# Optimization experiments

Measured on AMD Instinct MI355X. Metric: run time of the kernel, lower is better.

## Reference

```python
import jax, jax.numpy as jnp
import numpy as np

EPS = 1e-5
THRESH = 1.5


def _compute_one(x, g_w, g_b, phi_w, phi_b, W_w, W_b, gamma, beta):
    # x: (c, w, h, z) -- single sample (torch code calls compute_x with batch 1)
    c, w, h, z = x.shape
    nz = z // 2
    # AdaptiveAvgPool3d(1) on x.permute(0,4,2,3,1): mean over (w, h, c) per z-slice -> (z,)
    p = x.mean(axis=(0, 1, 2))
    xp = x * p[None, None, None, :]
    # 1x1x1 conv projections (note: self.theta is defined but unused in the original)
    g_x = jnp.einsum('ic,cwhz->iwhz', g_w, x) + g_b[:, None, None, None]
    phi_x = jnp.einsum('ic,cwhz->iwhz', phi_w, xp) + phi_b[:, None, None, None]
    # MaxPool3d kernel (1,1,2): non-overlapping max pairs along z
    g_x = g_x.reshape(-1, w, h, nz, 2).max(axis=-1)      # (ic, w, h, nz)
    phi_x = phi_x.reshape(-1, w, h, nz, 2).max(axis=-1)  # (ic, w, h, nz)
    # theta_x: (x*p).permute(0,2,3,4,1).view(w*h, z, c)
    theta = xp.transpose(1, 2, 3, 0).reshape(w * h, z, c)
    # phi: permute(0,2,3,1,4).view(w*h, ic, nz)
    phi_m = phi_x.transpose(1, 2, 0, 3).reshape(w * h, -1, nz)
    # g: permute(0,2,3,4,1).view(w*h, nz, ic)
    g_m = g_x.transpose(1, 2, 3, 0).reshape(w * h, nz, -1)
    f = jnp.einsum('bzc,bcn->bzn', theta, phi_m)          # (wh, z, nz)
    a = jax.nn.softmax(f, axis=-1)
    y = jnp.einsum('bzn,bni->bzi', a, g_m)                # (wh, z, ic)
    y = y.reshape(w, h, z, -1).transpose(3, 0, 1, 2)      # (ic, w, h, z)
    wy = jnp.einsum('ci,iwhz->cwhz', W_w, y) + W_b[:, None, None, None]
    # BatchNorm3d in training mode on a single-sample batch: per-channel stats over (w,h,z)
    mu = wy.mean(axis=(1, 2, 3), keepdims=True)
    var = wy.var(axis=(1, 2, 3), keepdims=True)
    wy = (wy - mu) * jax.lax.rsqrt(var + EPS)
    wy = wy * gamma[:, None, None, None] + beta[:, None, None, None]
    return wy + x


def setup_inputs() -> dict:
    key = jax.random.key(0)
    ks = jax.random.split(key, 10)
    b, c, w, h, z = 2, 64, 64, 64, 64
    ic = c  # inter_channels defaults to in_channels
    x = jax.random.normal(ks[0], (b, c, w, h, z), dtype=jnp.float32)
    # spacings in [0, 3): some samples fall above spacing_thresh=1.5 (identity branch)
    spacings = jax.random.uniform(ks[1], (b, 3), dtype=jnp.float32) * 3.0
    g_w = jax.random.normal(ks[2], (ic, c), dtype=jnp.float32) * 0.1
    g_b = jax.random.normal(ks[3], (ic,), dtype=jnp.float32) * 0.1
    phi_w = jax.random.normal(ks[4], (ic, c), dtype=jnp.float32) * 0.1
    phi_b = jax.random.normal(ks[5], (ic,), dtype=jnp.float32) * 0.1
    W_w = jax.random.normal(ks[6], (c, ic), dtype=jnp.float32) * 0.1
    W_b = jax.random.normal(ks[7], (c,), dtype=jnp.float32) * 0.1
    gamma = jax.random.normal(ks[8], (c,), dtype=jnp.float32) * 0.1
    beta = jax.random.normal(ks[9], (c,), dtype=jnp.float32) * 0.1
    return {"x": x, "spacings": spacings, "g_w": g_w, "g_b": g_b,
            "phi_w": phi_w, "phi_b": phi_b, "W_w": W_w, "W_b": W_b,
            "gamma": gamma, "beta": beta}


def reference(x, spacings, g_w, g_b, phi_w, phi_b, W_w, W_b, gamma, beta):
    out = jax.vmap(_compute_one, in_axes=(0,) + (None,) * 8)(
        x, g_w, g_b, phi_w, phi_b, W_w, W_b, gamma, beta)
    use = (spacings[:, -1] <= THRESH)[:, None, None, None, None]
    return jnp.where(use, out, x)
```

## Files before the change

kernel.cpp:

```cpp
#include <hip/hip_runtime.h>
#include <math.h>

#define THRESH_SP 1.5f
#define WHZc   262144
#define CWHZc  16777216

#define WS_PSUM   0
#define WS_SLOT   128
#define WS_ZERO_N 8320
#define WS_WY_BYTE 65536
#define WS_WY_NEED (WS_WY_BYTE + 2u * CWHZc * 2u)

typedef __attribute__((ext_vector_type(8))) short bf16x8;
typedef __attribute__((ext_vector_type(4))) float floatx4;

#define MFMA(a, b, c) __builtin_amdgcn_mfma_f32_16x16x32_bf16((a), (b), (c), 0, 0, 0)

__device__ __forceinline__ unsigned short f2b(float f) {
    unsigned int u = __builtin_bit_cast(unsigned int, f);
    return (unsigned short)((u + 0x7FFFu + ((u >> 16) & 1u)) >> 16);
}
__device__ __forceinline__ float b2f(unsigned short h) {
    unsigned int u = ((unsigned int)h) << 16;
    return __builtin_bit_cast(float, u);
}
__device__ __forceinline__ bf16x8 ldfrag(const unsigned short* p, int elem_off) {
    return *(const bf16x8*)(p + elem_off);
}

__global__ __launch_bounds__(256) void k_zero(float* __restrict__ ws) {
    int i = blockIdx.x * blockDim.x + threadIdx.x;
    if (i < WS_ZERO_N) ws[i] = 0.0f;
}

__global__ __launch_bounds__(256) void k_pmean(const float* __restrict__ x,
                                               const float* __restrict__ sp,
                                               float* __restrict__ ws) {
    const int b = blockIdx.x >> 9;
    if (sp[b*3 + 2] > THRESH_SP) return;
    const int jb = blockIdx.x & 511;
    __shared__ float s[64];
    const int t = threadIdx.x;
    if (t < 64) s[t] = 0.0f;
    __syncthreads();
    const int idx4 = jb * 256 + t;
    const int z0 = (idx4 & 15) * 4;
    float a0 = 0.f, a1 = 0.f, a2 = 0.f, a3 = 0.f;
    const float* xb = x + (size_t)b * CWHZc;
#pragma unroll 4
    for (int it = 0; it < 32; ++it) {
        const float4 v = *(const float4*)&xb[(size_t)(idx4 + it * 131072) * 4];
        a0 += v.x; a1 += v.y; a2 += v.z; a3 += v.w;
    }
    a0 += __shfl_xor(a0, 16); a0 += __shfl_xor(a0, 32);
    a1 += __shfl_xor(a1, 16); a1 += __shfl_xor(a1, 32);
    a2 += __shfl_xor(a2, 16); a2 += __shfl_xor(a2, 32);
    a3 += __shfl_xor(a3, 16); a3 += __shfl_xor(a3, 32);
    if ((t & 63) < 16) {
        unsafeAtomicAdd(&s[z0 + 0], a0);
        unsafeAtomicAdd(&s[z0 + 1], a1);
        unsafeAtomicAdd(&s[z0 + 2], a2);
        unsafeAtomicAdd(&s[z0 + 3], a3);
    }
    __syncthreads();
    if (t < 64) unsafeAtomicAdd(&ws[WS_PSUM + b * 64 + t], s[t]);
}

__global__ __launch_bounds__(256, 4) void k_main(
    const float* __restrict__ x, const float* __restrict__ sp,
    const float* __restrict__ gw, const float* __restrict__ gb,
    const float* __restrict__ pw, const float* __restrict__ pb,
    const float* __restrict__ Wwp, const float* __restrict__ Wbp,
    float* __restrict__ out, unsigned short* __restrict__ wy16, int use16,
    float* __restrict__ ws) {
    const int blk = blockIdx.x;
    const int b = blk >> 12;
    if (sp[b*3 + 2] > THRESH_SP) return;
    const int wh = blk & 4095;
    const int xbase = b * CWHZc + wh * 64;

    __shared__ unsigned short xT[64 * 72];
    __shared__ unsigned short wb[64 * 72];
    __shared__ unsigned short gpT[64 * 40];
    __shared__ unsigned short phpN[32 * 72];
    __shared__ unsigned short aT[64 * 40];
    __shared__ float p_s[64];

    const int t  = threadIdx.x;
    const int l  = t & 63;
    const int lr = l & 15;
    const int lq = l >> 4;
    const int zt = (t >> 6) << 4;

#pragma unroll
    for (int k = 0; k < 4; ++k) {
        const int f = t + (k << 8);
        const int c = f & 63, zq = f >> 6;
        const float4 v = *(const float4*)&x[xbase + c * WHZc + zq * 4];
        xT[(zq*4 + 0)*72 + c] = f2b(v.x);
        xT[(zq*4 + 1)*72 + c] = f2b(v.y);
        xT[(zq*4 + 2)*72 + c] = f2b(v.z);
        xT[(zq*4 + 3)*72 + c] = f2b(v.w);
    }
#pragma unroll
    for (int k = 0; k < 4; ++k) {
        const int f = t + (k << 8);
        const int i = f >> 4, c4 = f & 15;
        const float4 v = *(const float4*)&gw[i*64 + c4*4];
        uint2 pk;
        pk.x = (unsigned int)f2b(v.x) | ((unsigned int)f2b(v.y) << 16);
        pk.y = (unsigned int)f2b(v.z) | ((unsigned int)f2b(v.w) << 16);
        *(uint2*)&wb[i*72 + c4*4] = pk;
    }
    if (t < 64) p_s[t] = ws[WS_PSUM + b*64 + t] * (1.0f / 262144.0f);
    __syncthreads();

    const bf16x8 a0 = ldfrag(xT, (zt + lr)*72 + lq*8);
    const bf16x8 a1 = ldfrag(xT, (zt + lr)*72 + lq*8 + 32);
    const float pz0 = p_s[zt + lq*4 + 0], pz1 = p_s[zt + lq*4 + 1];
    const float pz2 = p_s[zt + lq*4 + 2], pz3 = p_s[zt + lq*4 + 3];

    {
        const int n0 = (zt >> 1) + lq*2;
#pragma unroll
        for (int ti = 0; ti < 4; ++ti) {
            const int i = ti*16 + lr;
            const float bv = gb[i];
            floatx4 acc = {bv, bv, bv, bv};
            acc = MFMA(a0, ldfrag(wb, i*72 + lq*8), acc);
            acc = MFMA(a1, ldfrag(wb, i*72 + lq*8 + 32), acc);
            unsigned int pk = (unsigned int)f2b(fmaxf(acc[0], acc[1])) |
                              ((unsigned int)f2b(fmaxf(acc[2], acc[3])) << 16);
            *(unsigned int*)&gpT[i*40 + n0] = pk;
        }
    }
    __syncthreads();

#pragma unroll
    for (int k = 0; k < 4; ++k) {
        const int f = t + (k << 8);
        const int i = f >> 4, c4 = f & 15;
        const float4 v = *(const float4*)&pw[i*64 + c4*4];
        uint2 pk;
        pk.x = (unsigned int)f2b(v.x) | ((unsigned int)f2b(v.y) << 16);
        pk.y = (unsigned int)f2b(v.z) | ((unsigned int)f2b(v.w) << 16);
        *(uint2*)&wb[i*72 + c4*4] = pk;
    }
    __syncthreads();

    {
        const int n0 = (zt >> 1) + lq*2;
#pragma unroll
        for (int ti = 0; ti < 4; ++ti) {
            const int i = ti*16 + lr;
            floatx4 acc = {0.f, 0.f, 0.f, 0.f};
            acc = MFMA(a0, ldfrag(wb, i*72 + lq*8), acc);
            acc = MFMA(a1, ldfrag(wb, i*72 + lq*8 + 32), acc);
            const float bv = pb[i];
            const float v0 = fmaf(acc[0], pz0, bv), v1 = fmaf(acc[1], pz1, bv);
            const float v2 = fmaf(acc[2], pz2, bv), v3 = fmaf(acc[3], pz3, bv);
            phpN[n0*72 + i]       = f2b(fmaxf(v0, v1));
            phpN[(n0 + 1)*72 + i] = f2b(fmaxf(v2, v3));
        }
    }
    __syncthreads();

    {
        floatx4 f0 = {0.f, 0.f, 0.f, 0.f}, f1 = {0.f, 0.f, 0.f, 0.f};
        f0 = MFMA(a0, ldfrag(phpN, lr*72 + lq*8), f0);
        f0 = MFMA(a1, ldfrag(phpN, lr*72 + lq*8 + 32), f0);
        f1 = MFMA(a0, ldfrag(phpN, (16 + lr)*72 + lq*8), f1);
        f1 = MFMA(a1, ldfrag(phpN, (16 + lr)*72 + lq*8 + 32), f1);
        const float pz[4] = {pz0, pz1, pz2, pz3};
#pragma unroll
        for (int r = 0; r < 4; ++r) {
            const float fr0 = f0[r] * pz[r], fr1 = f1[r] * pz[r];
            float m = fmaxf(fr0, fr1);
            m = fmaxf(m, __shfl_xor(m, 1)); m = fmaxf(m, __shfl_xor(m, 2));
            m = fmaxf(m, __shfl_xor(m, 4)); m = fmaxf(m, __shfl_xor(m, 8));
            const float e0 = __expf(fr0 - m), e1 = __expf(fr1 - m);
            float s = e0 + e1;
            s += __shfl_xor(s, 1); s += __shfl_xor(s, 2);
            s += __shfl_xor(s, 4); s += __shfl_xor(s, 8);
            const float inv = 1.0f / s;
            const int z = zt + lq*4 + r;
            aT[z*40 + lr]      = f2b(e0 * inv);
            aT[z*40 + lr + 16] = f2b(e1 * inv);
        }
#pragma unroll
        for (int k = 0; k < 4; ++k) {
            const int f = t + (k << 8);
            const int i = f >> 4, c4 = f & 15;
            const float4 v = *(const float4*)&Wwp[i*64 + c4*4];
            uint2 pk;
            pk.x = (unsigned int)f2b(v.x) | ((unsigned int)f2b(v.y) << 16);
            pk.y = (unsigned int)f2b(v.z) | ((unsigned int)f2b(v.w) << 16);
            *(uint2*)&wb[i*72 + c4*4] = pk;
        }
    }
    __syncthreads();

    {
        float* statsf = (float*)phpN;
        if (t < 128) statsf[t] = 0.0f;
        const bf16x8 av = ldfrag(aT, (zt + lr)*40 + lq*8);
#pragma unroll
        for (int ti = 0; ti < 4; ++ti) {
            floatx4 acc = {0.f, 0.f, 0.f, 0.f};
            acc = MFMA(av, ldfrag(gpT, (ti*16 + lr)*40 + lq*8), acc);
#pragma unroll
            for (int r = 0; r < 4; ++r)
                xT[(zt + lq*4 + r)*72 + ti*16 + lr] = f2b(acc[r]);
        }
    }
    __syncthreads();

    {
        float* statsf = (float*)phpN;
        const bf16x8 y0 = ldfrag(xT, (zt + lr)*72 + lq*8);
        const bf16x8 y1 = ldfrag(xT, (zt + lr)*72 + lq*8 + 32);
#pragma unroll
        for (int ti = 0; ti < 4; ++ti) {
            const int co = ti*16 + lr;
            const float bv = Wbp[co];
            floatx4 acc = {bv, bv, bv, bv};
            acc = MFMA(y0, ldfrag(wb, co*72 + lq*8), acc);
            acc = MFMA(y1, ldfrag(wb, co*72 + lq*8 + 32), acc);
            if (use16) {
                uint2 pk;
                pk.x = (unsigned int)f2b(acc[0]) | ((unsigned int)f2b(acc[1]) << 16);
                pk.y = (unsigned int)f2b(acc[2]) | ((unsigned int)f2b(acc[3]) << 16);
                *(uint2*)&wy16[(size_t)xbase + co * WHZc + zt + lq*4] = pk;
            } else {
                *(float4*)&out[xbase + co * WHZc + zt + lq*4] = *(float4*)&acc;
            }
            float s1 = acc[0] + acc[1] + acc[2] + acc[3];
            float s2 = acc[0]*acc[0] + acc[1]*acc[1] + acc[2]*acc[2] + acc[3]*acc[3];
            s1 += __shfl_xor(s1, 16); s1 += __shfl_xor(s1, 32);
            s2 += __shfl_xor(s2, 16); s2 += __shfl_xor(s2, 32);
            if (lq == 0) {
                atomicAdd(&statsf[co*2],     s1);
                atomicAdd(&statsf[co*2 + 1], s2);
            }
        }
    }
    __syncthreads();
    {
        const float* statsf = (const float*)phpN;
        if (t < 128) {
            const int slot = blk & 31;
            unsafeAtomicAdd(&ws[WS_SLOT + (slot*2 + b)*128 + t], statsf[t]);
        }
    }
}

__global__ __launch_bounds__(256) void k_final(const float* __restrict__ x,
                                               const float* __restrict__ sp,
                                               const float* __restrict__ gamma,
                                               const float* __restrict__ beta,
                                               float* __restrict__ out,
                                               const unsigned short* __restrict__ wy16,
                                               int use16,
                                               const float* __restrict__ ws) {
    const bool use0 = sp[2] <= THRESH_SP;
    const bool use1 = sp[5] <= THRESH_SP;
    __shared__ float scf[128], shf[128];
    if ((use0 || use1) && threadIdx.x < 128) {
        const int t = threadIdx.x;
        const int b = t >> 6, c = t & 63;
        float S1 = 0.f, S2 = 0.f;
        for (int s = 0; s < 32; s++) {
            S1 += ws[WS_SLOT + (s*2 + b)*128 + c*2 + 0];
            S2 += ws[WS_SLOT + (s*2 + b)*128 + c*2 + 1];
        }
        const float N = 262144.0f;
        const float mu = S1 / N;
        const float var = fmaxf(S2 / N - mu * mu, 0.0f);
        const float sc = gamma[c] * rsqrtf(var + 1e-5f);
        scf[t] = sc;
        shf[t] = beta[c] - mu * sc;
    }
    __syncthreads();
    const int nf4 = (2 * CWHZc) / 4;
    for (int i4 = blockIdx.x * blockDim.x + threadIdx.x; i4 < nf4;
         i4 += gridDim.x * blockDim.x) {
        const int idx = i4 * 4;
        const int b = idx >> 24;
        const bool use = b ? use1 : use0;
        const float4 xv = *(const float4*)&x[idx];
        float4 ov;
        if (use) {
            const int c = (idx >> 18) & 63;
            const float scv = scf[b * 64 + c];
            const float shv = shf[b * 64 + c];
            float w0, w1, w2, w3;
            if (use16) {
                const uint2 q = *(const uint2*)&wy16[idx];
                w0 = b2f((unsigned short)(q.x & 0xffffu));
                w1 = b2f((unsigned short)(q.x >> 16));
                w2 = b2f((unsigned short)(q.y & 0xffffu));
                w3 = b2f((unsigned short)(q.y >> 16));
            } else {
                const float4 wy = *(const float4*)&out[idx];
                w0 = wy.x; w1 = wy.y; w2 = wy.z; w3 = wy.w;
            }
            ov.x = w0 * scv + shv + xv.x;
            ov.y = w1 * scv + shv + xv.y;
            ov.z = w2 * scv + shv + xv.z;
            ov.w = w3 * scv + shv + xv.w;
        } else {
            ov = xv;
        }
        *(float4*)&out[idx] = ov;
    }
}

extern "C" void kernel_launch(void* const* d_in, const int* in_sizes, int n_in,
                              void* d_out, int out_size, void* d_ws, size_t ws_size,
                              hipStream_t stream) {
    const float* x     = (const float*)d_in[0];
    const float* spv   = (const float*)d_in[1];
    const float* gw    = (const float*)d_in[2];
    const float* gb    = (const float*)d_in[3];
    const float* pw    = (const float*)d_in[4];
    const float* pb    = (const float*)d_in[5];
    const float* Ww    = (const float*)d_in[6];
    const float* Wb    = (const float*)d_in[7];
    const float* gamma = (const float*)d_in[8];
    const float* beta  = (const float*)d_in[9];
    float* out = (float*)d_out;
    float* ws  = (float*)d_ws;
    const int use16 = (ws_size >= (size_t)WS_WY_NEED) ? 1 : 0;
    unsigned short* wy16 = (unsigned short*)((char*)d_ws + WS_WY_BYTE);

    k_zero<<<(WS_ZERO_N + 255) / 256, 256, 0, stream>>>(ws);
    k_pmean<<<1024, 256, 0, stream>>>(x, spv, ws);
    k_main<<<8192, 256, 0, stream>>>(x, spv, gw, gb, pw, pb, Ww, Wb,
                                     out, wy16, use16, ws);
    k_final<<<2048, 256, 0, stream>>>(x, spv, gamma, beta, out, wy16, use16, ws);
}
```

Baseline: 130.6 us.

## Stage a bf16 copy of x in the mean pass and pre-convert weights

The channel-mean kernel now also writes a bf16 copy of x to the workspace. The main kernel loads its x tile from that copy, and the final kernel reads the residual x from it too, cutting fp32 traffic in later stages. A small prep kernel converts the three weight matrices to bf16 once, so each block copies them directly instead of converting per block. The trade-offs are an extra write pass over x and a residual add done in bf16 precision, which may widen output error. Each path is used only when the workspace is large enough.

```diff
diff --git a/kernel.cpp b/kernel.cpp
--- a/kernel.cpp
+++ b/kernel.cpp
@@ -1,4 +1,5 @@
 #include <hip/hip_runtime.h>
+#include <hip/hip_bf16.h>
 #include <math.h>
 
 #define THRESH_SP 1.5f
@@ -8,8 +9,12 @@
 #define WS_PSUM   0
 #define WS_SLOT   128
 #define WS_ZERO_N 8320
-#define WS_WY_BYTE 65536
-#define WS_WY_NEED (WS_WY_BYTE + 2u * CWHZc * 2u)
+#define WS_W16_BYTE  65536
+#define WS_WY_BYTE   131072
+#define WS_X16_BYTE  (WS_WY_BYTE + 2u*CWHZc*2u)
+#define WS_W16_NEED  (WS_W16_BYTE + 3u*4096u*2u)
+#define WS_WY_NEED   (WS_WY_BYTE + 2u*CWHZc*2u)
+#define WS_X16_NEED  (WS_X16_BYTE + 2u*CWHZc*2u)
 
 typedef __attribute__((ext_vector_type(8))) short bf16x8;
 typedef __attribute__((ext_vector_type(4))) float floatx4;
@@ -17,8 +22,8 @@
 #define MFMA(a, b, c) __builtin_amdgcn_mfma_f32_16x16x32_bf16((a), (b), (c), 0, 0, 0)
 
 __device__ __forceinline__ unsigned short f2b(float f) {
-    unsigned int u = __builtin_bit_cast(unsigned int, f);
-    return (unsigned short)((u + 0x7FFFu + ((u >> 16) & 1u)) >> 16);
+    __hip_bfloat16 h = __float2bfloat16(f);
+    return __builtin_bit_cast(unsigned short, h);
 }
 __device__ __forceinline__ float b2f(unsigned short h) {
     unsigned int u = ((unsigned int)h) << 16;
@@ -28,14 +33,26 @@
     return *(const bf16x8*)(p + elem_off);
 }
 
-__global__ __launch_bounds__(256) void k_zero(float* __restrict__ ws) {
-    int i = blockIdx.x * blockDim.x + threadIdx.x;
+__global__ __launch_bounds__(256) void k_prep(const float* __restrict__ gw,
+                                              const float* __restrict__ pw,
+                                              const float* __restrict__ Ww,
+                                              float* __restrict__ ws,
+                                              unsigned short* __restrict__ w16,
+                                              int usew16) {
+    const int i = blockIdx.x * 256 + threadIdx.x;
     if (i < WS_ZERO_N) ws[i] = 0.0f;
+    if (usew16 && i < 4096) {
+        w16[i]        = f2b(gw[i]);
+        w16[4096 + i] = f2b(pw[i]);
+        w16[8192 + i] = f2b(Ww[i]);
+    }
 }
 
 __global__ __launch_bounds__(256) void k_pmean(const float* __restrict__ x,
                                                const float* __restrict__ sp,
-                                               float* __restrict__ ws) {
+                                               float* __restrict__ ws,
+                                               unsigned short* __restrict__ x16,
+                                               int usex16) {
     const int b = blockIdx.x >> 9;
     if (sp[b*3 + 2] > THRESH_SP) return;
     const int jb = blockIdx.x & 511;
@@ -47,10 +64,18 @@
     const int z0 = (idx4 & 15) * 4;
     float a0 = 0.f, a1 = 0.f, a2 = 0.f, a3 = 0.f;
     const float* xb = x + (size_t)b * CWHZc;
+    unsigned short* xo = x16 + (size_t)b * CWHZc;
 #pragma unroll 4
     for (int it = 0; it < 32; ++it) {
-        const float4 v = *(const float4*)&xb[(size_t)(idx4 + it * 131072) * 4];
+        const size_t e4 = (size_t)(idx4 + it * 131072);
+        const float4 v = *(const float4*)&xb[e4 * 4];
         a0 += v.x; a1 += v.y; a2 += v.z; a3 += v.w;
+        if (usex16) {
+            uint2 pk;
+            pk.x = (unsigned int)f2b(v.x) | ((unsigned int)f2b(v.y) << 16);
+            pk.y = (unsigned int)f2b(v.z) | ((unsigned int)f2b(v.w) << 16);
+            *(uint2*)&xo[e4 * 4] = pk;
+        }
     }
     a0 += __shfl_xor(a0, 16); a0 += __shfl_xor(a0, 32);
     a1 += __shfl_xor(a1, 16); a1 += __shfl_xor(a1, 32);
@@ -72,6 +97,8 @@
     const float* __restrict__ pw, const float* __restrict__ pb,
     const float* __restrict__ Wwp, const float* __restrict__ Wbp,
     float* __restrict__ out, unsigned short* __restrict__ wy16, int use16,
+    const unsigned short* __restrict__ w16, int usew16,
+    const unsigned short* __restrict__ x16, int usex16,
     float* __restrict__ ws) {
     const int blk = blockIdx.x;
     const int b = blk >> 12;
@@ -92,25 +119,47 @@
     const int lq = l >> 4;
     const int zt = (t >> 6) << 4;
 
-#pragma unroll
-    for (int k = 0; k < 4; ++k) {
-        const int f = t + (k << 8);
-        const int c = f & 63, zq = f >> 6;
-        const float4 v = *(const float4*)&x[xbase + c * WHZc + zq * 4];
-        xT[(zq*4 + 0)*72 + c] = f2b(v.x);
-        xT[(zq*4 + 1)*72 + c] = f2b(v.y);
-        xT[(zq*4 + 2)*72 + c] = f2b(v.z);
-        xT[(zq*4 + 3)*72 + c] = f2b(v.w);
-    }
-#pragma unroll
-    for (int k = 0; k < 4; ++k) {
-        const int f = t + (k << 8);
-        const int i = f >> 4, c4 = f & 15;
-        const float4 v = *(const float4*)&gw[i*64 + c4*4];
-        uint2 pk;
-        pk.x = (unsigned int)f2b(v.x) | ((unsigned int)f2b(v.y) << 16);
-        pk.y = (unsigned int)f2b(v.z) | ((unsigned int)f2b(v.w) << 16);
-        *(uint2*)&wb[i*72 + c4*4] = pk;
+    if (usex16) {
+        const unsigned short* xs = x16 + xbase;
+#pragma unroll
+        for (int k = 0; k < 2; ++k) {
+            const int f = t + (k << 8);
+            const int c = f >> 3, seg = f & 7;
+            uint4 q = *(const uint4*)&xs[c * WHZc + seg * 8];
+            const unsigned short* qs = (const unsigned short*)&q;
+#pragma unroll
+            for (int j = 0; j < 8; ++j) xT[(seg*8 + j)*72 + c] = qs[j];
+        }
+    } else {
+#pragma unroll
+        for (int k = 0; k < 4; ++k) {
+            const int f = t + (k << 8);
+            const int c = f & 63, zq = f >> 6;
+            const float4 v = *(const float4*)&x[xbase + c * WHZc + zq * 4];
+            xT[(zq*4 + 0)*72 + c] = f2b(v.x);
+            xT[(zq*4 + 1)*72 + c] = f2b(v.y);
+            xT[(zq*4 + 2)*72 + c] = f2b(v.z);
+            xT[(zq*4 + 3)*72 + c] = f2b(v.w);
+        }
+    }
+    if (usew16) {
+#pragma unroll
+        for (int k = 0; k < 2; ++k) {
+            const int f = t + (k << 8);
+            const int i = f >> 3, seg = f & 7;
+            *(uint4*)&wb[i*72 + seg*8] = *(const uint4*)&w16[i*64 + seg*8];
+        }
+    } else {
+#pragma unroll
+        for (int k = 0; k < 4; ++k) {
+            const int f = t + (k << 8);
+            const int i = f >> 4, c4 = f & 15;
+            const float4 v = *(const float4*)&gw[i*64 + c4*4];
+            uint2 pk;
+            pk.x = (unsigned int)f2b(v.x) | ((unsigned int)f2b(v.y) << 16);
+            pk.y = (unsigned int)f2b(v.z) | ((unsigned int)f2b(v.w) << 16);
+            *(uint2*)&wb[i*72 + c4*4] = pk;
+        }
     }
     if (t < 64) p_s[t] = ws[WS_PSUM + b*64 + t] * (1.0f / 262144.0f);
     __syncthreads();
@@ -136,15 +185,24 @@
     }
     __syncthreads();
 
-#pragma unroll
-    for (int k = 0; k < 4; ++k) {
-        const int f = t + (k << 8);
-        const int i = f >> 4, c4 = f & 15;
-        const float4 v = *(const float4*)&pw[i*64 + c4*4];
-        uint2 pk;
-        pk.x = (unsigned int)f2b(v.x) | ((unsigned int)f2b(v.y) << 16);
-        pk.y = (unsigned int)f2b(v.z) | ((unsigned int)f2b(v.w) << 16);
-        *(uint2*)&wb[i*72 + c4*4] = pk;
+    if (usew16) {
+#pragma unroll
+        for (int k = 0; k < 2; ++k) {
+            const int f = t + (k << 8);
+            const int i = f >> 3, seg = f & 7;
+            *(uint4*)&wb[i*72 + seg*8] = *(const uint4*)&w16[4096 + i*64 + seg*8];
+        }
+    } else {
+#pragma unroll
+        for (int k = 0; k < 4; ++k) {
+            const int f = t + (k << 8);
+            const int i = f >> 4, c4 = f & 15;
+            const float4 v = *(const float4*)&pw[i*64 + c4*4];
+            uint2 pk;
+            pk.x = (unsigned int)f2b(v.x) | ((unsigned int)f2b(v.y) << 16);
+            pk.y = (unsigned int)f2b(v.z) | ((unsigned int)f2b(v.w) << 16);
+            *(uint2*)&wb[i*72 + c4*4] = pk;
+        }
     }
     __syncthreads();
 
@@ -187,15 +245,24 @@
             aT[z*40 + lr]      = f2b(e0 * inv);
             aT[z*40 + lr + 16] = f2b(e1 * inv);
         }
-#pragma unroll
-        for (int k = 0; k < 4; ++k) {
-            const int f = t + (k << 8);
-            const int i = f >> 4, c4 = f & 15;
-            const float4 v = *(const float4*)&Wwp[i*64 + c4*4];
-            uint2 pk;
-            pk.x = (unsigned int)f2b(v.x) | ((unsigned int)f2b(v.y) << 16);
-            pk.y = (unsigned int)f2b(v.z) | ((unsigned int)f2b(v.w) << 16);
-            *(uint2*)&wb[i*72 + c4*4] = pk;
+        if (usew16) {
+#pragma unroll
+            for (int k = 0; k < 2; ++k) {
+                const int f = t + (k << 8);
+                const int i = f >> 3, seg = f & 7;
+                *(uint4*)&wb[i*72 + seg*8] = *(const uint4*)&w16[8192 + i*64 + seg*8];
+            }
+        } else {
+#pragma unroll
+            for (int k = 0; k < 4; ++k) {
+                const int f = t + (k << 8);
+                const int i = f >> 4, c4 = f & 15;
+                const float4 v = *(const float4*)&Wwp[i*64 + c4*4];
+                uint2 pk;
+                pk.x = (unsigned int)f2b(v.x) | ((unsigned int)f2b(v.y) << 16);
+                pk.y = (unsigned int)f2b(v.z) | ((unsigned int)f2b(v.w) << 16);
+                *(uint2*)&wb[i*72 + c4*4] = pk;
+            }
         }
     }
     __syncthreads();
@@ -261,6 +328,8 @@
                                                float* __restrict__ out,
                                                const unsigned short* __restrict__ wy16,
                                                int use16,
+                                               const unsigned short* __restrict__ x16,
+                                               int usex16,
                                                const float* __restrict__ ws) {
     const bool use0 = sp[2] <= THRESH_SP;
     const bool use1 = sp[5] <= THRESH_SP;
@@ -287,12 +356,22 @@
         const int idx = i4 * 4;
         const int b = idx >> 24;
         const bool use = b ? use1 : use0;
-        const float4 xv = *(const float4*)&x[idx];
         float4 ov;
         if (use) {
             const int c = (idx >> 18) & 63;
             const float scv = scf[b * 64 + c];
             const float shv = shf[b * 64 + c];
+            float x0, x1, x2, x3;
+            if (usex16) {
+                const uint2 q = *(const uint2*)&x16[idx];
+                x0 = b2f((unsigned short)(q.x & 0xffffu));
+                x1 = b2f((unsigned short)(q.x >> 16));
+                x2 = b2f((unsigned short)(q.y & 0xffffu));
+                x3 = b2f((unsigned short)(q.y >> 16));
+            } else {
+                const float4 xv = *(const float4*)&x[idx];
+                x0 = xv.x; x1 = xv.y; x2 = xv.z; x3 = xv.w;
+            }
             float w0, w1, w2, w3;
             if (use16) {
                 const uint2 q = *(const uint2*)&wy16[idx];
@@ -304,12 +383,12 @@
                 const float4 wy = *(const float4*)&out[idx];
                 w0 = wy.x; w1 = wy.y; w2 = wy.z; w3 = wy.w;
             }
-            ov.x = w0 * scv + shv + xv.x;
-            ov.y = w1 * scv + shv + xv.y;
-            ov.z = w2 * scv + shv + xv.z;
-            ov.w = w3 * scv + shv + xv.w;
+            ov.x = w0 * scv + shv + x0;
+            ov.y = w1 * scv + shv + x1;
+            ov.z = w2 * scv + shv + x2;
+            ov.w = w3 * scv + shv + x3;
         } else {
-            ov = xv;
+            ov = *(const float4*)&x[idx];
         }
         *(float4*)&out[idx] = ov;
     }
@@ -330,12 +409,17 @@
     const float* beta  = (const float*)d_in[9];
     float* out = (float*)d_out;
     float* ws  = (float*)d_ws;
-    const int use16 = (ws_size >= (size_t)WS_WY_NEED) ? 1 : 0;
+    const int usew16 = (ws_size >= (size_t)WS_W16_NEED) ? 1 : 0;
+    const int use16  = (ws_size >= (size_t)WS_WY_NEED) ? 1 : 0;
+    const int usex16 = (ws_size >= (size_t)WS_X16_NEED) ? 1 : 0;
+    unsigned short* w16  = (unsigned short*)((char*)d_ws + WS_W16_BYTE);
     unsigned short* wy16 = (unsigned short*)((char*)d_ws + WS_WY_BYTE);
-
-    k_zero<<<(WS_ZERO_N + 255) / 256, 256, 0, stream>>>(ws);
-    k_pmean<<<1024, 256, 0, stream>>>(x, spv, ws);
+    unsigned short* x16  = (unsigned short*)((char*)d_ws + WS_X16_BYTE);
+
+    k_prep<<<48, 256, 0, stream>>>(gw, pw, Ww, ws, w16, usew16);
+    k_pmean<<<1024, 256, 0, stream>>>(x, spv, ws, x16, usex16);
     k_main<<<8192, 256, 0, stream>>>(x, spv, gw, gb, pw, pb, Ww, Wb,
-                                     out, wy16, use16, ws);
-    k_final<<<2048, 256, 0, stream>>>(x, spv, gamma, beta, out, wy16, use16, ws);
-}
+                                     out, wy16, use16, w16, usew16, x16, usex16, ws);
+    k_final<<<2048, 256, 0, stream>>>(x, spv, gamma, beta, out, wy16, use16,
+                                      x16, usex16, ws);
+}
```

After: 141.2 us. 1.08x slower.

## Process two wh columns per block sharing pre-converted bf16 weights in LDS

Applied to the files above, without the earlier changes.

Weights for g, phi and W are converted to bf16 once in a prep kernel, and each 512-thread block of k_main now handles two wh positions that share the weight tiles in LDS. The phi weights get their own buffer, which removes one barrier, and the W weights are loaded during the softmax phase to overlap with compute. Biases are staged in shared memory. The aim is to cut redundant weight conversion and loading and to reduce synchronisation. The cost is higher LDS use per block (about 61 KB), which may limit how many blocks fit on a CU.

```diff
diff --git a/kernel.cpp b/kernel.cpp
--- a/kernel.cpp
+++ b/kernel.cpp
@@ -1,4 +1,5 @@
 #include <hip/hip_runtime.h>
+#include <hip/hip_bf16.h>
 #include <math.h>
 
 #define THRESH_SP 1.5f
@@ -8,8 +9,10 @@
 #define WS_PSUM   0
 #define WS_SLOT   128
 #define WS_ZERO_N 8320
-#define WS_WY_BYTE 65536
-#define WS_WY_NEED (WS_WY_BYTE + 2u * CWHZc * 2u)
+#define WS_W16_BYTE  65536
+#define WS_WY_BYTE   131072
+#define WS_W16_NEED  (WS_W16_BYTE + 3u*4096u*2u)
+#define WS_WY_NEED   (WS_WY_BYTE + 2u*CWHZc*2u)
 
 typedef __attribute__((ext_vector_type(8))) short bf16x8;
 typedef __attribute__((ext_vector_type(4))) float floatx4;
@@ -17,8 +20,8 @@
 #define MFMA(a, b, c) __builtin_amdgcn_mfma_f32_16x16x32_bf16((a), (b), (c), 0, 0, 0)
 
 __device__ __forceinline__ unsigned short f2b(float f) {
-    unsigned int u = __builtin_bit_cast(unsigned int, f);
-    return (unsigned short)((u + 0x7FFFu + ((u >> 16) & 1u)) >> 16);
+    __hip_bfloat16 h = __float2bfloat16(f);
+    return __builtin_bit_cast(unsigned short, h);
 }
 __device__ __forceinline__ float b2f(unsigned short h) {
     unsigned int u = ((unsigned int)h) << 16;
@@ -28,9 +31,19 @@
     return *(const bf16x8*)(p + elem_off);
 }
 
-__global__ __launch_bounds__(256) void k_zero(float* __restrict__ ws) {
-    int i = blockIdx.x * blockDim.x + threadIdx.x;
+__global__ __launch_bounds__(256) void k_prep(const float* __restrict__ gw,
+                                              const float* __restrict__ pw,
+                                              const float* __restrict__ Ww,
+                                              float* __restrict__ ws,
+                                              unsigned short* __restrict__ w16,
+                                              int usew16) {
+    const int i = blockIdx.x * 256 + threadIdx.x;
     if (i < WS_ZERO_N) ws[i] = 0.0f;
+    if (usew16 && i < 4096) {
+        w16[i]        = f2b(gw[i]);
+        w16[4096 + i] = f2b(pw[i]);
+        w16[8192 + i] = f2b(Ww[i]);
+    }
 }
 
 __global__ __launch_bounds__(256) void k_pmean(const float* __restrict__ x,
@@ -66,35 +79,59 @@
     if (t < 64) unsafeAtomicAdd(&ws[WS_PSUM + b * 64 + t], s[t]);
 }
 
-__global__ __launch_bounds__(256, 4) void k_main(
+#define L_WG     0
+#define L_WP     9216
+#define L_XA     18432
+#define L_GPA    27648
+#define L_PHA    32768
+#define L_XB     37376
+#define L_GPB    46592
+#define L_PHB    51712
+#define L_ATB    56320
+#define L_BIAS   61440
+#define L_PS     62208
+#define L_TOTAL  62464
+
+__global__ __launch_bounds__(512, 4) void k_main(
     const float* __restrict__ x, const float* __restrict__ sp,
     const float* __restrict__ gw, const float* __restrict__ gb,
     const float* __restrict__ pw, const float* __restrict__ pb,
     const float* __restrict__ Wwp, const float* __restrict__ Wbp,
     float* __restrict__ out, unsigned short* __restrict__ wy16, int use16,
+    const unsigned short* __restrict__ w16, int usew16,
     float* __restrict__ ws) {
     const int blk = blockIdx.x;
-    const int b = blk >> 12;
+    const int b = blk >> 11;
     if (sp[b*3 + 2] > THRESH_SP) return;
-    const int wh = blk & 4095;
+    const int whpair = (blk & 2047) * 2;
+
+    __shared__ char smem[L_TOTAL];
+    unsigned short* wg   = (unsigned short*)(smem + L_WG);
+    unsigned short* wp   = (unsigned short*)(smem + L_WP);
+    float*          bias = (float*)(smem + L_BIAS);
+    float*          p_s  = (float*)(smem + L_PS);
+    float*          statsf = (float*)(smem + L_PHA);
+
+    const int t   = threadIdx.x;
+    const int wv  = t >> 6;
+    const int cid = wv >> 2;
+    const int tt  = t & 255;
+    const int l   = t & 63;
+    const int lr  = l & 15;
+    const int lq  = l >> 4;
+    const int zt  = (wv & 3) << 4;
+
+    unsigned short* xT   = (unsigned short*)(smem + (cid ? L_XB  : L_XA));
+    unsigned short* gpT  = (unsigned short*)(smem + (cid ? L_GPB : L_GPA));
+    unsigned short* phpN = (unsigned short*)(smem + (cid ? L_PHB : L_PHA));
+    unsigned short* aT   = (unsigned short*)(smem + (cid ? L_ATB : L_WG));
+
+    const int wh    = whpair + cid;
     const int xbase = b * CWHZc + wh * 64;
 
-    __shared__ unsigned short xT[64 * 72];
-    __shared__ unsigned short wb[64 * 72];
-    __shared__ unsigned short gpT[64 * 40];
-    __shared__ unsigned short phpN[32 * 72];
-    __shared__ unsigned short aT[64 * 40];
-    __shared__ float p_s[64];
-
-    const int t  = threadIdx.x;
-    const int l  = t & 63;
-    const int lr = l & 15;
-    const int lq = l >> 4;
-    const int zt = (t >> 6) << 4;
-
 #pragma unroll
     for (int k = 0; k < 4; ++k) {
-        const int f = t + (k << 8);
+        const int f = tt + (k << 8);
         const int c = f & 63, zq = f >> 6;
         const float4 v = *(const float4*)&x[xbase + c * WHZc + zq * 4];
         xT[(zq*4 + 0)*72 + c] = f2b(v.x);
@@ -102,17 +139,32 @@
         xT[(zq*4 + 2)*72 + c] = f2b(v.z);
         xT[(zq*4 + 3)*72 + c] = f2b(v.w);
     }
-#pragma unroll
-    for (int k = 0; k < 4; ++k) {
-        const int f = t + (k << 8);
-        const int i = f >> 4, c4 = f & 15;
-        const float4 v = *(const float4*)&gw[i*64 + c4*4];
-        uint2 pk;
-        pk.x = (unsigned int)f2b(v.x) | ((unsigned int)f2b(v.y) << 16);
-        pk.y = (unsigned int)f2b(v.z) | ((unsigned int)f2b(v.w) << 16);
-        *(uint2*)&wb[i*72 + c4*4] = pk;
-    }
-    if (t < 64) p_s[t] = ws[WS_PSUM + b*64 + t] * (1.0f / 262144.0f);
+    if (usew16) {
+#pragma unroll
+        for (int k = 0; k < 2; ++k) {
+            const int f = t + (k << 9);
+            const int mat = f >> 9;
+            const int i = (f & 511) >> 3, seg = f & 7;
+            unsigned short* dst = mat ? wp : wg;
+            *(uint4*)&dst[i*72 + seg*8] = *(const uint4*)&w16[mat*4096 + i*64 + seg*8];
+        }
+    } else {
+#pragma unroll
+        for (int k = 0; k < 4; ++k) {
+            const int f = t + (k << 9);
+            const int mat = f >> 10, ff = f & 1023;
+            const int i = ff >> 4, c4 = ff & 15;
+            const float* src = mat ? pw : gw;
+            unsigned short* dst = mat ? wp : wg;
+            const float4 v = *(const float4*)&src[i*64 + c4*4];
+            uint2 pk;
+            pk.x = (unsigned)f2b(v.x) | ((unsigned)f2b(v.y) << 16);
+            pk.y = (unsigned)f2b(v.z) | ((unsigned)f2b(v.w) << 16);
+            *(uint2*)&dst[i*72 + c4*4] = pk;
+        }
+    }
+    if (t < 192) bias[t] = (t < 64) ? gb[t] : (t < 128) ? pb[t - 64] : Wbp[t - 128];
+    if (t < 64)  p_s[t] = ws[WS_PSUM + b*64 + t] * (1.0f / 262144.0f);
     __syncthreads();
 
     const bf16x8 a0 = ldfrag(xT, (zt + lr)*72 + lq*8);
@@ -125,26 +177,14 @@
 #pragma unroll
         for (int ti = 0; ti < 4; ++ti) {
             const int i = ti*16 + lr;
-            const float bv = gb[i];
+            const float bv = bias[i];
             floatx4 acc = {bv, bv, bv, bv};
-            acc = MFMA(a0, ldfrag(wb, i*72 + lq*8), acc);
-            acc = MFMA(a1, ldfrag(wb, i*72 + lq*8 + 32), acc);
-            unsigned int pk = (unsigned int)f2b(fmaxf(acc[0], acc[1])) |
-                              ((unsigned int)f2b(fmaxf(acc[2], acc[3])) << 16);
+            acc = MFMA(a0, ldfrag(wg, i*72 + lq*8), acc);
+            acc = MFMA(a1, ldfrag(wg, i*72 + lq*8 + 32), acc);
+            unsigned int pk = (unsigned)f2b(fmaxf(acc[0], acc[1])) |
+                              ((unsigned)f2b(fmaxf(acc[2], acc[3])) << 16);
             *(unsigned int*)&gpT[i*40 + n0] = pk;
         }
-    }
-    __syncthreads();
-
-#pragma unroll
-    for (int k = 0; k < 4; ++k) {
-        const int f = t + (k << 8);
-        const int i = f >> 4, c4 = f & 15;
-        const float4 v = *(const float4*)&pw[i*64 + c4*4];
-        uint2 pk;
-        pk.x = (unsigned int)f2b(v.x) | ((unsigned int)f2b(v.y) << 16);
-        pk.y = (unsigned int)f2b(v.z) | ((unsigned int)f2b(v.w) << 16);
-        *(uint2*)&wb[i*72 + c4*4] = pk;
     }
     __syncthreads();
 
@@ -154,9 +194,9 @@
         for (int ti = 0; ti < 4; ++ti) {
             const int i = ti*16 + lr;
             floatx4 acc = {0.f, 0.f, 0.f, 0.f};
-            acc = MFMA(a0, ldfrag(wb, i*72 + lq*8), acc);
-            acc = MFMA(a1, ldfrag(wb, i*72 + lq*8 + 32), acc);
-            const float bv = pb[i];
+            acc = MFMA(a0, ldfrag(wp, i*72 + lq*8), acc);
+            acc = MFMA(a1, ldfrag(wp, i*72 + lq*8 + 32), acc);
+            const float bv = bias[64 + i];
             const float v0 = fmaf(acc[0], pz0, bv), v1 = fmaf(acc[1], pz1, bv);
             const float v2 = fmaf(acc[2], pz2, bv), v3 = fmaf(acc[3], pz3, bv);
             phpN[n0*72 + i]       = f2b(fmaxf(v0, v1));
@@ -171,6 +211,21 @@
         f0 = MFMA(a1, ldfrag(phpN, lr*72 + lq*8 + 32), f0);
         f1 = MFMA(a0, ldfrag(phpN, (16 + lr)*72 + lq*8), f1);
         f1 = MFMA(a1, ldfrag(phpN, (16 + lr)*72 + lq*8 + 32), f1);
+        if (usew16) {
+            const int i = t >> 3, seg = t & 7;
+            *(uint4*)&wp[i*72 + seg*8] = *(const uint4*)&w16[8192 + i*64 + seg*8];
+        } else {
+#pragma unroll
+            for (int k = 0; k < 2; ++k) {
+                const int f = t + (k << 9);
+                const int i = f >> 4, c4 = f & 15;
+                const float4 v = *(const float4*)&Wwp[i*64 + c4*4];
+                uint2 pk;
+                pk.x = (unsigned)f2b(v.x) | ((unsigned)f2b(v.y) << 16);
+                pk.y = (unsigned)f2b(v.z) | ((unsigned)f2b(v.w) << 16);
+                *(uint2*)&wp[i*72 + c4*4] = pk;
+            }
+        }
         const float pz[4] = {pz0, pz1, pz2, pz3};
 #pragma unroll
         for (int r = 0; r < 4; ++r) {
@@ -187,21 +242,10 @@
             aT[z*40 + lr]      = f2b(e0 * inv);
             aT[z*40 + lr + 16] = f2b(e1 * inv);
         }
-#pragma unroll
-        for (int k = 0; k < 4; ++k) {
-            const int f = t + (k << 8);
-            const int i = f >> 4, c4 = f & 15;
-            const float4 v = *(const float4*)&Wwp[i*64 + c4*4];
-            uint2 pk;
-            pk.x = (unsigned int)f2b(v.x) | ((unsigned int)f2b(v.y) << 16);
-            pk.y = (unsigned int)f2b(v.z) | ((unsigned int)f2b(v.w) << 16);
-            *(uint2*)&wb[i*72 + c4*4] = pk;
-        }
-    }
-    __syncthreads();
-
-    {
-        float* statsf = (float*)phpN;
+    }
+    __syncthreads();
+
+    {
         if (t < 128) statsf[t] = 0.0f;
         const bf16x8 av = ldfrag(aT, (zt + lr)*40 + lq*8);
 #pragma unroll
@@ -216,20 +260,19 @@
     __syncthreads();
 
     {
-        float* statsf = (float*)phpN;
         const bf16x8 y0 = ldfrag(xT, (zt + lr)*72 + lq*8);
         const bf16x8 y1 = ldfrag(xT, (zt + lr)*72 + lq*8 + 32);
 #pragma unroll
         for (int ti = 0; ti < 4; ++ti) {
             const int co = ti*16 + lr;
-            const float bv = Wbp[co];
+            const float bv = bias[128 + co];
             floatx4 acc = {bv, bv, bv, bv};
-            acc = MFMA(y0, ldfrag(wb, co*72 + lq*8), acc);
-            acc = MFMA(y1, ldfrag(wb, co*72 + lq*8 + 32), acc);
+            acc = MFMA(y0, ldfrag(wp, co*72 + lq*8), acc);
+            acc = MFMA(y1, ldfrag(wp, co*72 + lq*8 + 32), acc);
             if (use16) {
                 uint2 pk;
-                pk.x = (unsigned int)f2b(acc[0]) | ((unsigned int)f2b(acc[1]) << 16);
-                pk.y = (unsigned int)f2b(acc[2]) | ((unsigned int)f2b(acc[3]) << 16);
+                pk.x = (unsigned)f2b(acc[0]) | ((unsigned)f2b(acc[1]) << 16);
+                pk.y = (unsigned)f2b(acc[2]) | ((unsigned)f2b(acc[3]) << 16);
                 *(uint2*)&wy16[(size_t)xbase + co * WHZc + zt + lq*4] = pk;
             } else {
                 *(float4*)&out[xbase + co * WHZc + zt + lq*4] = *(float4*)&acc;
@@ -245,12 +288,9 @@
         }
     }
     __syncthreads();
-    {
-        const float* statsf = (const float*)phpN;
-        if (t < 128) {
-            const int slot = blk & 31;
-            unsafeAtomicAdd(&ws[WS_SLOT + (slot*2 + b)*128 + t], statsf[t]);
-        }
+    if (t < 128) {
+        const int slot = blk & 31;
+        unsafeAtomicAdd(&ws[WS_SLOT + (slot*2 + b)*128 + t], statsf[t]);
     }
 }
 
@@ -330,12 +370,14 @@
     const float* beta  = (const float*)d_in[9];
     float* out = (float*)d_out;
     float* ws  = (float*)d_ws;
-    const int use16 = (ws_size >= (size_t)WS_WY_NEED) ? 1 : 0;
+    const int usew16 = (ws_size >= (size_t)WS_W16_NEED) ? 1 : 0;
+    const int use16  = (ws_size >= (size_t)WS_WY_NEED) ? 1 : 0;
+    unsigned short* w16  = (unsigned short*)((char*)d_ws + WS_W16_BYTE);
     unsigned short* wy16 = (unsigned short*)((char*)d_ws + WS_WY_BYTE);
 
-    k_zero<<<(WS_ZERO_N + 255) / 256, 256, 0, stream>>>(ws);
+    k_prep<<<48, 256, 0, stream>>>(gw, pw, Ww, ws, w16, usew16);
     k_pmean<<<1024, 256, 0, stream>>>(x, spv, ws);
-    k_main<<<8192, 256, 0, stream>>>(x, spv, gw, gb, pw, pb, Ww, Wb,
-                                     out, wy16, use16, ws);
+    k_main<<<4096, 512, 0, stream>>>(x, spv, gw, gb, pw, pb, Ww, Wb,
+                                     out, wy16, use16, w16, usew16, ws);
     k_final<<<2048, 256, 0, stream>>>(x, spv, gamma, beta, out, wy16, use16, ws);
 }
```

After: 130.6 us. About the same (+0.1%).
